# Performance work log

Measured on AMD Instinct MI355X. Metric: run time of the kernel, lower is better.

The kernel has to match this reference:

```python
import jax, jax.numpy as jnp
import numpy as np

# Module hyperparameters (from init_kwargs)
B = 8          # batch_size
NV = 8192      # num_template_vertices
NS = 4096      # num_fixed_samples
NPD = 64       # round(NS ** 0.5)
L_BOUND = 0.0
U_BOUND = 1.0
BD = (U_BOUND - L_BOUND) / (NPD - 1)   # min_sigma default
D_DIM = 2.0
C = (4.0 / (D_DIM + 2)) ** (1.0 / (D_DIM + 4)) * NV ** (-1.0 / (D_DIM + 4))
CF = (2.0 * np.pi) ** (-D_DIM / 2) / C ** D_DIM
CN = -1.0 / (2.0 * C ** 2)


def _make_grid():
    g = jnp.linspace(L_BOUND, U_BOUND, NPD, dtype=jnp.float32)
    gx, gy = jnp.meshgrid(g, g, indexing='ij')          # torch.meshgrid default 'ij'
    S = jnp.stack([gx, gy], axis=-1).reshape(NPD * NPD, 2)
    return jnp.broadcast_to(S[None], (B, NPD * NPD, 2))  # [B, npd^2, 2]


def setup_inputs() -> dict:
    key = jax.random.key(0)
    T = jax.random.uniform(key, (B, NV, 2), dtype=jnp.float32)  # UV in [0,1]
    S = _make_grid()
    return {"T": T, "S": S}


def reference(T, S):
    # sigma: per-batch bandwidth from vertex spread (torch std is unbiased, ddof=1)
    sigma = jnp.clip(jnp.std(T, axis=1, ddof=1).mean(axis=-1), BD)  # [B]
    # batched squared-L2 cdist: D[b,i,j] = ||S[b,i] - T[b,j]||^2  -> [B, npd^2, nV]
    s2 = jnp.sum(S * S, axis=-1)[:, :, None]
    t2 = jnp.sum(T * T, axis=-1)[:, None, :]
    cross = jnp.einsum('bik,bjk->bij', S, T)
    D = s2 + t2 - 2.0 * cross
    # Gaussian kernel density estimate at each grid point, mean over vertices
    E = jnp.exp(CN * D / (sigma[:, None, None] ** 2))
    K_H = CF * sigma[:, None] ** (-D_DIM) * E.mean(axis=-1)    # [B, npd^2]
    # normalize to a histogram
    return K_H / jnp.clip(K_H.sum(axis=1, keepdims=True), 1e-05)
```

## Files before the change

kernel.cpp:

```cpp
#include <hip/hip_runtime.h>
#include <math.h>

#define BATCH 8
#define NVERT 8192
#define NPD   64
#define NCELL 4096
#define SPLITS 64
#define JPB   (NVERT / SPLITS)
#define G     16

#ifndef M_PI
#define M_PI 3.14159265358979323846
#endif

#define PARAMS_OFF   0
#define TOTPART_OFF  16
#define PARTIALS_OFF 1024

static __device__ __forceinline__ float fast_exp2(float x) {
#if __has_builtin(__builtin_amdgcn_exp2f)
    return __builtin_amdgcn_exp2f(x);
#else
    return exp2f(x);
#endif
}

__global__ __launch_bounds__(256) void kde_kernel(const float* __restrict__ T,
                                                  float* __restrict__ params,
                                                  float* __restrict__ totpart,
                                                  float* __restrict__ partials) {
    const int b   = blockIdx.x >> 6;
    const int sp  = blockIdx.x & (SPLITS - 1);
    const int j0  = sp * JPB;
    const int tid = threadIdx.x;

    __shared__ float  es[G][128];
    __shared__ float2 tj[JPB];
    __shared__ float  red[4][4];
    __shared__ float  bcast[2];

    const float2* Tb = reinterpret_cast<const float2*>(T) + (size_t)b * NVERT;
    float sx = 0.f, sx2 = 0.f, sy = 0.f, sy2 = 0.f;
    for (int j = tid; j < NVERT; j += 256) {
        float2 v = Tb[j];
        sx += v.x; sx2 = fmaf(v.x, v.x, sx2);
        sy += v.y; sy2 = fmaf(v.y, v.y, sy2);
        int local = j - j0;
        if ((unsigned)local < (unsigned)JPB) tj[local] = v;
    }
    for (int off = 32; off; off >>= 1) {
        sx  += __shfl_down(sx,  off);  sx2 += __shfl_down(sx2, off);
        sy  += __shfl_down(sy,  off);  sy2 += __shfl_down(sy2, off);
    }
    const int w = tid >> 6, lane = tid & 63;
    if (lane == 0) { red[w][0] = sx; red[w][1] = sx2; red[w][2] = sy; red[w][3] = sy2; }
    __syncthreads();
    if (tid == 0) {
        double tsx = 0, tsx2 = 0, tsy = 0, tsy2 = 0;
        for (int i = 0; i < 4; ++i) {
            tsx += red[i][0]; tsx2 += red[i][1]; tsy += red[i][2]; tsy2 += red[i][3];
        }
        const double N = (double)NVERT;
        double varx = (tsx2 - tsx * tsx / N) / (N - 1.0);
        double vary = (tsy2 - tsy * tsy / N) / (N - 1.0);
        double sigma = 0.5 * (sqrt(varx) + sqrt(vary));
        const double BD = 1.0 / 63.0;
        if (sigma < BD) sigma = BD;
        const double C2 = pow(2.0, -13.0 / 3.0);
        double s2 = sigma * sigma;
        bcast[0] = (float)(-0.5 / C2 / (s2 * 0.69314718055994530942));
        bcast[1] = (float)(1.0 / (2.0 * M_PI * C2) / (s2 * N));
        if (sp == 0) params[b] = bcast[1];
    }
    __syncthreads();
    const float kexp2 = bcast[0];

    const int tx = tid & 15;
    const int ty = tid >> 4;
    float acc[4][4];
#pragma unroll
    for (int i = 0; i < 4; ++i)
#pragma unroll
        for (int j = 0; j < 4; ++j) acc[i][j] = 0.0f;

    for (int jg = 0; jg < JPB; jg += G) {
        __syncthreads();
#pragma unroll
        for (int r = 0; r < 8; ++r) {
            int idx = r * 256 + tid;
            int g = idx >> 7, c = idx & 127;
            float2 t2 = tj[jg + g];
            float tv = (c < 64) ? t2.x : t2.y;
            float d = (float)(c & 63) * (1.0f / 63.0f) - tv;
            es[g][c] = fast_exp2(kexp2 * d * d);
        }
        __syncthreads();
#pragma unroll
        for (int g = 0; g < G; ++g) {
            float4 ex = *reinterpret_cast<const float4*>(&es[g][tx * 4]);
            float4 ey = *reinterpret_cast<const float4*>(&es[g][64 + ty * 4]);
            acc[0][0] += ex.x * ey.x; acc[0][1] += ex.x * ey.y;
            acc[0][2] += ex.x * ey.z; acc[0][3] += ex.x * ey.w;
            acc[1][0] += ex.y * ey.x; acc[1][1] += ex.y * ey.y;
            acc[1][2] += ex.y * ey.z; acc[1][3] += ex.y * ey.w;
            acc[2][0] += ex.z * ey.x; acc[2][1] += ex.z * ey.y;
            acc[2][2] += ex.z * ey.z; acc[2][3] += ex.z * ey.w;
            acc[3][0] += ex.w * ey.x; acc[3][1] += ex.w * ey.y;
            acc[3][2] += ex.w * ey.z; acc[3][3] += ex.w * ey.w;
        }
    }

    float* dst = partials + (size_t)blockIdx.x * NCELL;
    float tsum = 0.f;
#pragma unroll
    for (int i = 0; i < 4; ++i) {
        float4 v = make_float4(acc[i][0], acc[i][1], acc[i][2], acc[i][3]);
        *reinterpret_cast<float4*>(&dst[(tx * 4 + i) * 64 + ty * 4]) = v;
        tsum += (acc[i][0] + acc[i][1]) + (acc[i][2] + acc[i][3]);
    }
    for (int off = 32; off; off >>= 1) tsum += __shfl_down(tsum, off);
    __syncthreads();
    if (lane == 0) red[w][0] = tsum;
    __syncthreads();
    if (tid == 0) totpart[blockIdx.x] = (red[0][0] + red[1][0]) + (red[2][0] + red[3][0]);
}

__global__ __launch_bounds__(256) void finish_kernel(const float* __restrict__ partials,
                                                     const float* __restrict__ totpart,
                                                     const float* __restrict__ params,
                                                     float* __restrict__ out) {
    const int b    = blockIdx.x >> 4;
    const int cell = ((blockIdx.x & 15) << 8) + threadIdx.x;
    const float* p = partials + (size_t)(b * SPLITS) * NCELL + cell;
    float s0 = 0.f, s1 = 0.f, s2 = 0.f, s3 = 0.f;
#pragma unroll
    for (int k = 0; k < SPLITS; k += 4) {
        s0 += p[(size_t)(k + 0) * NCELL];
        s1 += p[(size_t)(k + 1) * NCELL];
        s2 += p[(size_t)(k + 2) * NCELL];
        s3 += p[(size_t)(k + 3) * NCELL];
    }
    float s = (s0 + s1) + (s2 + s3);

    __shared__ float tot_s;
    if (threadIdx.x < 64) {
        float v = totpart[(b << 6) + threadIdx.x];
        for (int off = 32; off; off >>= 1) v += __shfl_down(v, off);
        if (threadIdx.x == 0) tot_s = v;
    }
    __syncthreads();
    const float scale = params[b];
    const float denom = fmaxf(tot_s * scale, 1e-5f);
    out[b * NCELL + cell] = (s * scale) / denom;
}

extern "C" void kernel_launch(void* const* d_in, const int* in_sizes, int n_in,
                              void* d_out, int out_size, void* d_ws, size_t ws_size,
                              hipStream_t stream) {
    const float* T = (const float*)d_in[0];

    float* ws       = (float*)d_ws;
    float* params   = ws + PARAMS_OFF;
    float* totpart  = ws + TOTPART_OFF;
    float* partials = ws + PARTIALS_OFF;

    kde_kernel<<<BATCH * SPLITS, 256, 0, stream>>>(T, params, totpart, partials);
    finish_kernel<<<BATCH * 16, 256, 0, stream>>>(partials, totpart, params, (float*)d_out);
}
```

Measured before the change: 80.31 us.

## Split vertex groups per wave with 8x8 register tiles and double-buffered staging

Each wavefront now handles its own subset of vertex rows and accumulates all 4096 cells as an 8x8 per-lane register tile. This raises reuse of the LDS exp values and removes the cross-wave reduction. The exp staging is double-buffered, which drops one barrier per round, and T is loaded as float4. The cost is that every wave writes its own partial histogram, so partial-buffer writes and the finish kernel's reads grow fourfold. The larger accumulator tile also raises register pressure.

```diff
diff --git a/kernel.cpp b/kernel.cpp
--- a/kernel.cpp
+++ b/kernel.cpp
@@ -8,6 +8,8 @@
 #define SPLITS 64
 #define JPB   (NVERT / SPLITS)
 #define G     16
+#define ROUNDS (JPB / G)
+#define SLICES 256
 
 #ifndef M_PI
 #define M_PI 3.14159265358979323846
@@ -15,7 +17,7 @@
 
 #define PARAMS_OFF   0
 #define TOTPART_OFF  16
-#define PARTIALS_OFF 1024
+#define PARTIALS_OFF 4096
 
 static __device__ __forceinline__ float fast_exp2(float x) {
 #if __has_builtin(__builtin_amdgcn_exp2f)
@@ -33,26 +35,30 @@
     const int sp  = blockIdx.x & (SPLITS - 1);
     const int j0  = sp * JPB;
     const int tid = threadIdx.x;
+    const int w    = tid >> 6;
+    const int lane = tid & 63;
 
-    __shared__ float  es[G][128];
+    __shared__ float  es[2][G][128];
     __shared__ float2 tj[JPB];
     __shared__ float  red[4][4];
     __shared__ float  bcast[2];
 
-    const float2* Tb = reinterpret_cast<const float2*>(T) + (size_t)b * NVERT;
+    const float4* T4 = reinterpret_cast<const float4*>(T + (size_t)b * NVERT * 2);
     float sx = 0.f, sx2 = 0.f, sy = 0.f, sy2 = 0.f;
-    for (int j = tid; j < NVERT; j += 256) {
-        float2 v = Tb[j];
-        sx += v.x; sx2 = fmaf(v.x, v.x, sx2);
-        sy += v.y; sy2 = fmaf(v.y, v.y, sy2);
-        int local = j - j0;
-        if ((unsigned)local < (unsigned)JPB) tj[local] = v;
+    for (int q = tid; q < NVERT / 2; q += 256) {
+        float4 v = T4[q];
+        sx += v.x + v.z;
+        sy += v.y + v.w;
+        sx2 += v.x * v.x + v.z * v.z;
+        sy2 += v.y * v.y + v.w * v.w;
+        int local = 2 * q - j0;
+        if ((unsigned)local < (unsigned)JPB)
+            *reinterpret_cast<float4*>(&tj[local]) = v;
     }
     for (int off = 32; off; off >>= 1) {
         sx  += __shfl_down(sx,  off);  sx2 += __shfl_down(sx2, off);
         sy  += __shfl_down(sy,  off);  sy2 += __shfl_down(sy2, off);
     }
-    const int w = tid >> 6, lane = tid & 63;
     if (lane == 0) { red[w][0] = sx; red[w][1] = sx2; red[w][2] = sy; red[w][3] = sy2; }
     __syncthreads();
     if (tid == 0) {
@@ -75,54 +81,67 @@
     __syncthreads();
     const float kexp2 = bcast[0];
 
-    const int tx = tid & 15;
-    const int ty = tid >> 4;
-    float acc[4][4];
+    const int   c     = tid & 127;
+    const bool  isX   = (c < 64);
+    const float xc    = (float)(c & 63) * (1.0f / 63.0f);
+    const int   gbase = tid >> 7;
+
+#define STAGE(JG, BUF)                                                    \
+    {                                                                     \
+        _Pragma("unroll")                                                 \
+        for (int r_ = 0; r_ < 8; ++r_) {                                  \
+            int g = r_ * 2 + gbase;                                       \
+            float2 t2 = tj[(JG) + g];                                     \
+            float tv = isX ? t2.x : t2.y;                                 \
+            float d = xc - tv;                                            \
+            es[BUF][g][c] = fast_exp2(kexp2 * d * d);                     \
+        }                                                                 \
+    }
+
+    const int tx = lane >> 3;
+    const int ty = lane & 7;
+    float acc[8][8];
 #pragma unroll
-    for (int i = 0; i < 4; ++i)
+    for (int i = 0; i < 8; ++i)
 #pragma unroll
-        for (int j = 0; j < 4; ++j) acc[i][j] = 0.0f;
+        for (int j = 0; j < 8; ++j) acc[i][j] = 0.0f;
 
-    for (int jg = 0; jg < JPB; jg += G) {
+    STAGE(0, 0);
+    for (int r = 0; r < ROUNDS; ++r) {
         __syncthreads();
+        if (r + 1 < ROUNDS) STAGE((r + 1) * G, (r + 1) & 1);
+        const float (*E)[128] = es[r & 1];
 #pragma unroll
-        for (int r = 0; r < 8; ++r) {
-            int idx = r * 256 + tid;
-            int g = idx >> 7, c = idx & 127;
-            float2 t2 = tj[jg + g];
-            float tv = (c < 64) ? t2.x : t2.y;
-            float d = (float)(c & 63) * (1.0f / 63.0f) - tv;
-            es[g][c] = fast_exp2(kexp2 * d * d);
-        }
-        __syncthreads();
+        for (int v = 0; v < 4; ++v) {
+            const float* row = E[(w << 2) + v];
+            float4 ex0 = *reinterpret_cast<const float4*>(&row[tx * 8]);
+            float4 ex1 = *reinterpret_cast<const float4*>(&row[tx * 8 + 4]);
+            float4 ey0 = *reinterpret_cast<const float4*>(&row[64 + ty * 8]);
+            float4 ey1 = *reinterpret_cast<const float4*>(&row[64 + ty * 8 + 4]);
+            float ex[8] = {ex0.x, ex0.y, ex0.z, ex0.w, ex1.x, ex1.y, ex1.z, ex1.w};
+            float ey[8] = {ey0.x, ey0.y, ey0.z, ey0.w, ey1.x, ey1.y, ey1.z, ey1.w};
 #pragma unroll
-        for (int g = 0; g < G; ++g) {
-            float4 ex = *reinterpret_cast<const float4*>(&es[g][tx * 4]);
-            float4 ey = *reinterpret_cast<const float4*>(&es[g][64 + ty * 4]);
-            acc[0][0] += ex.x * ey.x; acc[0][1] += ex.x * ey.y;
-            acc[0][2] += ex.x * ey.z; acc[0][3] += ex.x * ey.w;
-            acc[1][0] += ex.y * ey.x; acc[1][1] += ex.y * ey.y;
-            acc[1][2] += ex.y * ey.z; acc[1][3] += ex.y * ey.w;
-            acc[2][0] += ex.z * ey.x; acc[2][1] += ex.z * ey.y;
-            acc[2][2] += ex.z * ey.z; acc[2][3] += ex.z * ey.w;
-            acc[3][0] += ex.w * ey.x; acc[3][1] += ex.w * ey.y;
-            acc[3][2] += ex.w * ey.z; acc[3][3] += ex.w * ey.w;
+            for (int i = 0; i < 8; ++i)
+#pragma unroll
+                for (int j = 0; j < 8; ++j)
+                    acc[i][j] = fmaf(ex[i], ey[j], acc[i][j]);
         }
     }
 
-    float* dst = partials + (size_t)blockIdx.x * NCELL;
+    float* dst = partials + ((size_t)blockIdx.x * 4 + w) * NCELL;
     float tsum = 0.f;
 #pragma unroll
-    for (int i = 0; i < 4; ++i) {
-        float4 v = make_float4(acc[i][0], acc[i][1], acc[i][2], acc[i][3]);
-        *reinterpret_cast<float4*>(&dst[(tx * 4 + i) * 64 + ty * 4]) = v;
-        tsum += (acc[i][0] + acc[i][1]) + (acc[i][2] + acc[i][3]);
+    for (int i = 0; i < 8; ++i) {
+        float4 lo = make_float4(acc[i][0], acc[i][1], acc[i][2], acc[i][3]);
+        float4 hi = make_float4(acc[i][4], acc[i][5], acc[i][6], acc[i][7]);
+        int rowoff = (tx * 8 + i) * 64 + ty * 8;
+        *reinterpret_cast<float4*>(&dst[rowoff])     = lo;
+        *reinterpret_cast<float4*>(&dst[rowoff + 4]) = hi;
+        tsum += ((acc[i][0] + acc[i][1]) + (acc[i][2] + acc[i][3]))
+              + ((acc[i][4] + acc[i][5]) + (acc[i][6] + acc[i][7]));
     }
     for (int off = 32; off; off >>= 1) tsum += __shfl_down(tsum, off);
-    __syncthreads();
-    if (lane == 0) red[w][0] = tsum;
-    __syncthreads();
-    if (tid == 0) totpart[blockIdx.x] = (red[0][0] + red[1][0]) + (red[2][0] + red[3][0]);
+    if (lane == 0) totpart[(size_t)blockIdx.x * 4 + w] = tsum;
 }
 
 __global__ __launch_bounds__(256) void finish_kernel(const float* __restrict__ partials,
@@ -131,10 +150,9 @@
                                                      float* __restrict__ out) {
     const int b    = blockIdx.x >> 4;
     const int cell = ((blockIdx.x & 15) << 8) + threadIdx.x;
-    const float* p = partials + (size_t)(b * SPLITS) * NCELL + cell;
+    const float* p = partials + (size_t)b * SLICES * NCELL + cell;
     float s0 = 0.f, s1 = 0.f, s2 = 0.f, s3 = 0.f;
-#pragma unroll
-    for (int k = 0; k < SPLITS; k += 4) {
+    for (int k = 0; k < SLICES; k += 4) {
         s0 += p[(size_t)(k + 0) * NCELL];
         s1 += p[(size_t)(k + 1) * NCELL];
         s2 += p[(size_t)(k + 2) * NCELL];
@@ -142,15 +160,15 @@
     }
     float s = (s0 + s1) + (s2 + s3);
 
-    __shared__ float tot_s;
-    if (threadIdx.x < 64) {
-        float v = totpart[(b << 6) + threadIdx.x];
-        for (int off = 32; off; off >>= 1) v += __shfl_down(v, off);
-        if (threadIdx.x == 0) tot_s = v;
-    }
+    __shared__ float r4[4];
+    float v = totpart[b * SLICES + threadIdx.x];
+    for (int off = 32; off; off >>= 1) v += __shfl_down(v, off);
+    if ((threadIdx.x & 63) == 0) r4[threadIdx.x >> 6] = v;
     __syncthreads();
+    const float tot = (r4[0] + r4[1]) + (r4[2] + r4[3]);
+
     const float scale = params[b];
-    const float denom = fmaxf(tot_s * scale, 1e-5f);
+    const float denom = fmaxf(tot * scale, 1e-5f);
     out[b * NCELL + cell] = (s * scale) / denom;
 }
 
```

After: 100.4 us. 1.25x slower.
